# Optimization experiments

Measured on AMD Instinct MI355X. Metric: run time of the kernel, lower is better.

Reference implementation:

```python
import jax, jax.numpy as jnp
import numpy as np
from jax import lax

B, L, C, H, W = 4, 64, 64, 32, 32
K = 3
CONN = 4


def _conv(x, w, b):
    # x: (N, C_in, H, W), w: (C_out, C_in, K, K) -- stride 1, pad K//2 (same as nn.Conv2d)
    p = K // 2
    y = lax.conv_general_dilated(x, w, window_strides=(1, 1), padding=[(p, p), (p, p)],
                                 dimension_numbers=("NCHW", "OIHW", "NCHW"))
    return y + b[None, :, None, None]


def _neighbours_sum(n, m):
    # n: (B*L, C, H, W); m: (B, L, L) bool adjacency with CONN True per row.
    # Equivalent to masked_select + view(B,L,CONN,C,H,W).sum(2): a masked neighbor sum.
    nb = n.reshape(B, L, C, H, W)
    o = jnp.einsum("bij,bjchw->bichw", m.astype(n.dtype), nb)
    return o.reshape(B * L, C, H, W)


def setup_inputs() -> dict:
    key = jax.random.key(0)
    ks = jax.random.split(key, 9)
    fan0 = 1.0 / np.sqrt(C * K * K)
    x = jax.random.normal(ks[0], (B * L, C, H, W), dtype=jnp.float32)
    w_x0 = jax.random.uniform(ks[1], (C, C, K, K), jnp.float32, -fan0, fan0)
    b_x0 = jax.random.uniform(ks[2], (C,), jnp.float32, -fan0, fan0)
    w_n0 = jax.random.uniform(ks[3], (C, C, K, K), jnp.float32, -fan0, fan0)
    b_n0 = jax.random.uniform(ks[4], (C,), jnp.float32, -fan0, fan0)
    w_x1 = jax.random.uniform(ks[5], (C, C, K, K), jnp.float32, -fan0, fan0)
    b_x1 = jax.random.uniform(ks[6], (C,), jnp.float32, -fan0, fan0)
    w_n1 = jax.random.uniform(ks[7], (C, C, K, K), jnp.float32, -fan0, fan0)
    b_n1 = jax.random.uniform(ks[8], (C,), jnp.float32, -fan0, fan0)
    # adjacency with exactly CONN neighbors per (b, i) row
    rng = np.random.default_rng(0)
    idx = np.argsort(rng.random((B, L, L)), axis=-1)[..., :CONN]
    mask = np.zeros((B, L, L), dtype=bool)
    np.put_along_axis(mask, idx, True, axis=-1)
    return {"x": x, "w_x0": w_x0, "b_x0": b_x0, "w_n0": w_n0, "b_n0": b_n0,
            "w_x1": w_x1, "b_x1": b_x1, "w_n1": w_n1, "b_n1": b_n1,
            "neighbours_matrix": jnp.asarray(mask), "connected_num": 4}


def reference(x, w_x0, b_x0, w_n0, b_n0, w_x1, b_x1, w_n1, b_n1, neighbours_matrix, connected_num):
    residual = x
    n_set = _conv(x, w_n0, b_n0)
    h = _conv(x, w_x0, b_x0)
    h = jax.nn.relu(h + _neighbours_sum(n_set, neighbours_matrix))
    n_set = _conv(h, w_n1, b_n1)
    h2 = _conv(h, w_x1, b_x1)
    h2 = h2 + _neighbours_sum(n_set, neighbours_matrix)
    return jax.nn.relu(h2 + residual)
```

## Files before the change

### kernel.cpp

```cpp
#include <hip/hip_runtime.h>

#define NIMG 256
#define CCH 64
#define HWSZ 1024
#define IMG_NHWC 65536

typedef __attribute__((ext_vector_type(8))) short  s16x8;
typedef __attribute__((ext_vector_type(4))) short  s16x4;
typedef __attribute__((ext_vector_type(4))) float  f32x4;

__device__ __forceinline__ unsigned short f2bf(float f) {
    unsigned u = __builtin_bit_cast(unsigned, f);
    u += 0x7fffu + ((u >> 16) & 1u);
    return (unsigned short)(u >> 16);
}
__device__ __forceinline__ float bf2f(unsigned short h) {
    unsigned u = ((unsigned)h) << 16;
    return __builtin_bit_cast(float, u);
}

__device__ __forceinline__ void gload_lds16(const void* g, void* l) {
    __builtin_amdgcn_global_load_lds(
        (const __attribute__((address_space(1))) unsigned int*)g,
        (__attribute__((address_space(3))) unsigned int*)l, 16, 0, 0);
}

__global__ __launch_bounds__(256) void build_nbr_kernel(const unsigned char* __restrict__ mraw,
                                                        int* __restrict__ nbr) {
    __shared__ int nz;
    int t = threadIdx.x;
    if (t == 0) nz = 0;
    __syncthreads();
    int local = 0;
    for (int i = t; i < 16384; i += 256) local += (mraw[i] != 0) ? 1 : 0;
    atomicAdd(&nz, local);
    __syncthreads();
    bool isByte = (nz == 1024);
    const int* mi = (const int*)mraw;
    int c = 0;
    int base = t * 64;
    for (int j = 0; j < 64; ++j) {
        int v = isByte ? (int)mraw[base + j] : mi[base + j];
        if (v != 0 && c < 4) { nbr[t * 4 + c] = j; ++c; }
    }
    for (; c < 4; ++c) nbr[t * 4 + c] = -1;
}

__global__ __launch_bounds__(256) void pack_w_kernel(const float* __restrict__ w0,
                                                     const float* __restrict__ w1,
                                                     const float* __restrict__ w2,
                                                     const float* __restrict__ w3,
                                                     unsigned short* __restrict__ wp) {
    int idx = blockIdx.x * 256 + threadIdx.x;
    if (idx >= 147456) return;
    int e  = idx & 7;
    int sp = (idx >> 3) & 7;
    int co = (idx >> 6) & 63;
    int tc = idx >> 12;
    int cv = tc / 9, tap = tc - cv * 9;
    int ci = ((sp ^ (co & 7)) << 3) + e;
    const float* w = (cv == 0) ? w0 : (cv == 1) ? w1 : (cv == 2) ? w2 : w3;
    wp[idx] = f2bf(w[(co * 64 + ci) * 9 + tap]);
}

__global__ __launch_bounds__(256) void to_nhwc_kernel(const float* __restrict__ x,
                                                      unsigned short* __restrict__ xb) {
    __shared__ unsigned short lds[256 * 68];
    int bid = blockIdx.x;
    int n = bid >> 2, px0 = (bid & 3) * 256;
    int t = threadIdx.x, w = t >> 6, l = t & 63;

    #pragma unroll
    for (int pp = 0; pp < 8; ++pp) {
        int c = w * 16 + pp * 2;
        const float* s0 = x + ((size_t)(n * 64 + c)) * HWSZ + px0;
        const float* s1 = s0 + HWSZ;
        #pragma unroll
        for (int ch = 0; ch < 4; ++ch) {
            int px = ch * 64 + l;
            unsigned pack = (unsigned)f2bf(s0[px]) | ((unsigned)f2bf(s1[px]) << 16);
            *(unsigned*)((char*)lds + px * 136 + c * 2) = pack;
        }
    }
    __syncthreads();
    #pragma unroll
    for (int it = 0; it < 8; ++it) {
        int pos = it * 256 + t;
        int px = pos >> 3, c0 = (pos & 7) * 8;
        const char* src = (const char*)lds + px * 136 + c0 * 2;
        s16x4 v0 = *(const s16x4*)src;
        s16x4 v1 = *(const s16x4*)(src + 8);
        unsigned short* dst = xb + ((size_t)(n * 1024) + px0 + px) * 64 + c0;
        *(s16x4*)dst = v0;
        *(s16x4*)(dst + 4) = v1;
    }
}

__global__ __launch_bounds__(256, 1) void conv_mfma_kernel(const unsigned short* __restrict__ act,
                                                           const unsigned short* __restrict__ wconv,
                                                           const float* __restrict__ bias,
                                                           unsigned short* __restrict__ outp) {
    __shared__ unsigned short wlds[36864];
    __shared__ unsigned short inb[2][10 * 34 * 64];
    int n = blockIdx.x;
    int t = threadIdx.x, w = t >> 6, l = t & 63;

    const unsigned short* img = act + ((size_t)n << 16);
    int x1 = (t >> 3) & 31, slot = t & 7;
    int c = x1 + 1;
    int sslot = slot ^ (c & 7);

    #pragma unroll
    for (int j = 0; j < 18; ++j) {
        int off = j * 4096 + w * 1024;
        gload_lds16((const char*)wconv + off + l * 16, (char*)wlds + off);
    }
    {
        char* ldsbase = (char*)inb[0] + (w * 8 + 1) * 128;
        #pragma unroll
        for (int r = 0; r < 10; ++r) {
            int y = -1 + r;
            if (y >= 0) {
                gload_lds16(img + (y * 32 + x1) * 64 + sslot * 8, ldsbase + r * 4352);
            } else {
                s16x8 z = {0,0,0,0,0,0,0,0};
                *(s16x8*)((char*)inb[0] + r * 4352 + c * 128 + slot * 16) = z;
            }
        }
        if (t < 160) {
            int r = t >> 4, cp = ((t >> 3) & 1) ? 33 : 0, sl = t & 7;
            s16x8 z = {0,0,0,0,0,0,0,0};
            int off = ((r * 34 + cp) * 128 + sl * 16) ^ ((cp & 7) << 4);
            *(s16x8*)((char*)inb[0] + off) = z;
            *(s16x8*)((char*)inb[1] + off) = z;
        }
    }
    __syncthreads();

    int lm = l & 15, kg = l >> 4;

    #pragma unroll
    for (int s = 0; s < 4; ++s) {
        if (s < 3) {
            int y0n = (s + 1) * 8;
            char* ldsbase = (char*)inb[(s + 1) & 1] + (w * 8 + 1) * 128;
            #pragma unroll
            for (int r = 0; r < 10; ++r) {
                int y = y0n - 1 + r;
                if (y < 32) {
                    gload_lds16(img + (y * 32 + x1) * 64 + sslot * 8, ldsbase + r * 4352);
                } else {
                    s16x8 z = {0,0,0,0,0,0,0,0};
                    *(s16x8*)((char*)inb[(s + 1) & 1] + r * 4352 + c * 128 + slot * 16) = z;
                }
            }
        }

        const char* tile = (const char*)inb[s & 1];
        f32x4 acc[4][4];
        #pragma unroll
        for (int m = 0; m < 4; ++m)
            #pragma unroll
            for (int p = 0; p < 4; ++p) acc[m][p] = (f32x4){0.f, 0.f, 0.f, 0.f};

        #pragma unroll
        for (int tap = 0; tap < 9; ++tap) {
            const int dy = tap / 3, dx = tap % 3;
            #pragma unroll
            for (int g = 0; g < 2; ++g) {
                s16x8 a[4], bfr[4];
                #pragma unroll
                for (int m = 0; m < 4; ++m) {
                    int row = m * 16 + lm;
                    int ao  = tap * 8192 + row * 128 + (((g * 4 + kg) ^ (lm & 7)) * 16);
                    a[m] = *(const s16x8*)((const char*)wlds + ao);
                }
                #pragma unroll
                for (int p = 0; p < 4; ++p) {
                    int r  = 2 * w + (p >> 1) + dy;
                    int xl = (p & 1) * 16 + lm + dx;
                    int lb = (r * 4352 + xl * 128 + g * 64 + kg * 16) ^ ((xl & 7) << 4);
                    bfr[p] = *(const s16x8*)(tile + lb);
                }
                #pragma unroll
                for (int m = 0; m < 4; ++m)
                    #pragma unroll
                    for (int p = 0; p < 4; ++p)
                        acc[m][p] = __builtin_amdgcn_mfma_f32_16x16x32_bf16(a[m], bfr[p], acc[m][p], 0, 0, 0);
            }
        }

        int y0 = s * 8;
        #pragma unroll
        for (int m = 0; m < 4; ++m) {
            f32x4 bv = *(const f32x4*)(bias + m * 16 + kg * 4);
            #pragma unroll
            for (int p = 0; p < 4; ++p) {
                int y  = y0 + 2 * w + (p >> 1);
                int xx = (p & 1) * 16 + lm;
                s16x4 o;
                #pragma unroll
                for (int j = 0; j < 4; ++j) o[j] = (short)f2bf(acc[m][p][j] + bv[j]);
                *(s16x4*)(outp + (((size_t)n * 1024 + y * 32 + xx) * 64) + m * 16 + kg * 4) = o;
            }
        }
        if (s < 3) __syncthreads();
    }
}

__global__ __launch_bounds__(256) void agg_relu_kernel(unsigned short* __restrict__ hx,
                                                       const unsigned short* __restrict__ nset,
                                                       const int* __restrict__ nbr) {
    int bid = blockIdx.x;
    int n = bid >> 5;
    int b = n >> 6;
    int rem = ((bid & 31) << 8) + threadIdx.x;
    size_t u = (((size_t)n) << 13) + rem;
    s16x8 hv = *(const s16x8*)(hx + u * 8);
    float s[8];
    #pragma unroll
    for (int j = 0; j < 8; ++j) s[j] = bf2f((unsigned short)hv[j]);
    #pragma unroll
    for (int k = 0; k < 4; ++k) {
        int jn = nbr[n * 4 + k];
        if (jn >= 0) {
            s16x8 nv = *(const s16x8*)(nset + ((((size_t)(b * 64 + jn)) << 13) + rem) * 8);
            #pragma unroll
            for (int j = 0; j < 8; ++j) s[j] += bf2f((unsigned short)nv[j]);
        }
    }
    s16x8 o;
    #pragma unroll
    for (int j = 0; j < 8; ++j) o[j] = (short)f2bf(fmaxf(s[j], 0.f));
    *(s16x8*)(hx + u * 8) = o;
}

__global__ __launch_bounds__(256) void final_kernel(const unsigned short* __restrict__ h2x,
                                                    const unsigned short* __restrict__ nset,
                                                    const int* __restrict__ nbr,
                                                    const float* __restrict__ x,
                                                    float* __restrict__ out) {
    __shared__ float lds[128 * 68];
    int bid = blockIdx.x;
    int n = bid >> 3, px0 = (bid & 7) * 128;
    int b = n >> 6;
    int t = threadIdx.x;
    int j0 = nbr[n * 4 + 0], j1 = nbr[n * 4 + 1], j2 = nbr[n * 4 + 2], j3 = nbr[n * 4 + 3];
    size_t base = ((size_t)n * 1024 + px0) * 64;
    size_t nb[4];
    nb[0] = ((size_t)(b * 64 + (j0 < 0 ? 0 : j0)) * 1024 + px0) * 64;
    nb[1] = ((size_t)(b * 64 + (j1 < 0 ? 0 : j1)) * 1024 + px0) * 64;
    nb[2] = ((size_t)(b * 64 + (j2 < 0 ? 0 : j2)) * 1024 + px0) * 64;
    nb[3] = ((size_t)(b * 64 + (j3 < 0 ? 0 : j3)) * 1024 + px0) * 64;
    int use[4] = {j0 >= 0, j1 >= 0, j2 >= 0, j3 >= 0};

    #pragma unroll
    for (int it = 0; it < 4; ++it) {
        int pos = it * 256 + t;
        int px = pos >> 3, c0 = (pos & 7) * 8;
        int off = px * 64 + c0;
        float s[8];
        s16x8 hv = *(const s16x8*)(h2x + base + off);
        #pragma unroll
        for (int j = 0; j < 8; ++j) s[j] = bf2f((unsigned short)hv[j]);
        #pragma unroll
        for (int k = 0; k < 4; ++k) {
            if (use[k]) {
                s16x8 nv = *(const s16x8*)(nset + nb[k] + off);
                #pragma unroll
                for (int j = 0; j < 8; ++j) s[j] += bf2f((unsigned short)nv[j]);
            }
        }
        float* dst = &lds[px * 68 + c0];
        *(f32x4*)dst = (f32x4){s[0], s[1], s[2], s[3]};
        *(f32x4*)(dst + 4) = (f32x4){s[4], s[5], s[6], s[7]};
    }
    __syncthreads();

    int w = t >> 6, l = t & 63;
    #pragma unroll
    for (int q = 0; q < 4; ++q) {
        int c0 = w * 16 + q * 4;
        #pragma unroll
        for (int half = 0; half < 2; ++half) {
            int px = half * 64 + l;
            f32x4 v = *(const f32x4*)&lds[px * 68 + c0];
            #pragma unroll
            for (int j = 0; j < 4; ++j) {
                size_t a = ((size_t)(n * 64) + c0 + j) * HWSZ + px0 + px;
                out[a] = fmaxf(v[j] + x[a], 0.f);
            }
        }
    }
}

extern "C" void kernel_launch(void* const* d_in, const int* in_sizes, int n_in,
                              void* d_out, int out_size, void* d_ws, size_t ws_size,
                              hipStream_t stream) {
    const float* x    = (const float*)d_in[0];
    const float* w_x0 = (const float*)d_in[1];
    const float* b_x0 = (const float*)d_in[2];
    const float* w_n0 = (const float*)d_in[3];
    const float* b_n0 = (const float*)d_in[4];
    const float* w_x1 = (const float*)d_in[5];
    const float* b_x1 = (const float*)d_in[6];
    const float* w_n1 = (const float*)d_in[7];
    const float* b_n1 = (const float*)d_in[8];
    const unsigned char* mask = (const unsigned char*)d_in[9];

    unsigned short* xb    = (unsigned short*)d_ws;
    unsigned short* hxb   = xb  + (size_t)NIMG * IMG_NHWC;
    unsigned short* nsetb = hxb + (size_t)NIMG * IMG_NHWC;
    unsigned short* wpack = nsetb + (size_t)NIMG * IMG_NHWC;
    int* nbr = (int*)(wpack + 147456);

    build_nbr_kernel<<<1, 256, 0, stream>>>(mask, nbr);
    pack_w_kernel<<<576, 256, 0, stream>>>(w_n0, w_x0, w_n1, w_x1, wpack);
    to_nhwc_kernel<<<1024, 256, 0, stream>>>(x, xb);

    const unsigned short* wp_n0 = wpack;
    const unsigned short* wp_x0 = wpack + 36864;
    const unsigned short* wp_n1 = wpack + 73728;
    const unsigned short* wp_x1 = wpack + 110592;

    conv_mfma_kernel<<<256, 256, 0, stream>>>(xb, wp_n0, b_n0, nsetb);
    conv_mfma_kernel<<<256, 256, 0, stream>>>(xb, wp_x0, b_x0, hxb);
    agg_relu_kernel<<<8192, 256, 0, stream>>>(hxb, nsetb, nbr);

    conv_mfma_kernel<<<256, 256, 0, stream>>>(hxb, wp_n1, b_n1, nsetb);
    conv_mfma_kernel<<<256, 256, 0, stream>>>(hxb, wp_x1, b_x1, xb);
    final_kernel<<<2048, 256, 0, stream>>>(xb, nsetb, nbr, x, (float*)d_out);
}
```

Baseline: 318.8 us.

## Merge conv pairs into one launch split by half-image, restage aggregation through LDS

Each layer's two convolutions run in a single launch with four times as many blocks, each handling a 16-row half image for one weight set, to fill more compute units. Neighbour aggregation now loads all 64 images' slices into LDS once per batch slice. The final kernel takes the residual from the bf16 NHWC copy instead of fp32 x. Weight packing and neighbour-list building share one launch. Halo rows are loaded twice and the bf16 residual reduces precision.

```diff
diff --git a/kernel.cpp b/kernel.cpp
--- a/kernel.cpp
+++ b/kernel.cpp
@@ -25,34 +25,34 @@
         (__attribute__((address_space(3))) unsigned int*)l, 16, 0, 0);
 }
 
-__global__ __launch_bounds__(256) void build_nbr_kernel(const unsigned char* __restrict__ mraw,
-                                                        int* __restrict__ nbr) {
-    __shared__ int nz;
-    int t = threadIdx.x;
-    if (t == 0) nz = 0;
-    __syncthreads();
-    int local = 0;
-    for (int i = t; i < 16384; i += 256) local += (mraw[i] != 0) ? 1 : 0;
-    atomicAdd(&nz, local);
-    __syncthreads();
-    bool isByte = (nz == 1024);
-    const int* mi = (const int*)mraw;
-    int c = 0;
-    int base = t * 64;
-    for (int j = 0; j < 64; ++j) {
-        int v = isByte ? (int)mraw[base + j] : mi[base + j];
-        if (v != 0 && c < 4) { nbr[t * 4 + c] = j; ++c; }
-    }
-    for (; c < 4; ++c) nbr[t * 4 + c] = -1;
-}
-
-__global__ __launch_bounds__(256) void pack_w_kernel(const float* __restrict__ w0,
-                                                     const float* __restrict__ w1,
-                                                     const float* __restrict__ w2,
-                                                     const float* __restrict__ w3,
-                                                     unsigned short* __restrict__ wp) {
+__global__ __launch_bounds__(256) void pack_build_kernel(const float* __restrict__ w0,
+                                                         const float* __restrict__ w1,
+                                                         const float* __restrict__ w2,
+                                                         const float* __restrict__ w3,
+                                                         unsigned short* __restrict__ wp,
+                                                         const unsigned char* __restrict__ mraw,
+                                                         int* __restrict__ nbr) {
+    if (blockIdx.x == 576) {
+        __shared__ int nz;
+        int t = threadIdx.x;
+        if (t == 0) nz = 0;
+        __syncthreads();
+        int local = 0;
+        for (int i = t; i < 16384; i += 256) local += (mraw[i] != 0) ? 1 : 0;
+        atomicAdd(&nz, local);
+        __syncthreads();
+        bool isByte = (nz == 1024);
+        const int* mi = (const int*)mraw;
+        int c = 0;
+        int base = t * 64;
+        for (int j = 0; j < 64; ++j) {
+            int v = isByte ? (int)mraw[base + j] : mi[base + j];
+            if (v != 0 && c < 4) { nbr[t * 4 + c] = j; ++c; }
+        }
+        for (; c < 4; ++c) nbr[t * 4 + c] = -1;
+        return;
+    }
     int idx = blockIdx.x * 256 + threadIdx.x;
-    if (idx >= 147456) return;
     int e  = idx & 7;
     int sp = (idx >> 3) & 7;
     int co = (idx >> 6) & 63;
@@ -96,19 +96,22 @@
     }
 }
 
-__global__ __launch_bounds__(256, 1) void conv_mfma_kernel(const unsigned short* __restrict__ act,
-                                                           const unsigned short* __restrict__ wconv,
-                                                           const float* __restrict__ bias,
-                                                           unsigned short* __restrict__ outp) {
+__global__ __launch_bounds__(256, 1) void conv_pair_kernel(const unsigned short* __restrict__ act,
+                                                           const unsigned short* __restrict__ wpA,
+                                                           const unsigned short* __restrict__ wpB,
+                                                           const float* __restrict__ bA,
+                                                           const float* __restrict__ bB,
+                                                           unsigned short* __restrict__ outA,
+                                                           unsigned short* __restrict__ outB) {
     __shared__ unsigned short wlds[36864];
-    __shared__ unsigned short inb[2][10 * 34 * 64];
-    int n = blockIdx.x;
+    __shared__ unsigned short tile[18 * 34 * 64];
+    int bid = blockIdx.x;
+    int n = bid >> 2, half = (bid >> 1) & 1, sel = bid & 1;
+    const unsigned short* wconv = sel ? wpB : wpA;
+    const float* bias = sel ? bB : bA;
+    unsigned short* outp = sel ? outB : outA;
+    int y0 = half * 16;
     int t = threadIdx.x, w = t >> 6, l = t & 63;
-
-    const unsigned short* img = act + ((size_t)n << 16);
-    int x1 = (t >> 3) & 31, slot = t & 7;
-    int c = x1 + 1;
-    int sslot = slot ^ (c & 7);
 
     #pragma unroll
     for (int j = 0; j < 18; ++j) {
@@ -116,129 +119,147 @@
         gload_lds16((const char*)wconv + off + l * 16, (char*)wlds + off);
     }
     {
-        char* ldsbase = (char*)inb[0] + (w * 8 + 1) * 128;
-        #pragma unroll
-        for (int r = 0; r < 10; ++r) {
-            int y = -1 + r;
-            if (y >= 0) {
-                gload_lds16(img + (y * 32 + x1) * 64 + sslot * 8, ldsbase + r * 4352);
+        const unsigned short* img = act + ((size_t)n << 16);
+        int x1 = (t >> 3) & 31, slot = t & 7;
+        int c = x1 + 1;
+        int sslot = slot ^ (c & 7);
+        char* base = (char*)tile + 128 + w * 1024;
+        #pragma unroll
+        for (int r = 0; r < 18; ++r) {
+            int y = y0 - 1 + r;
+            if (y >= 0 && y < 32) {
+                gload_lds16(img + (y * 32 + x1) * 64 + sslot * 8, base + r * 4352);
             } else {
                 s16x8 z = {0,0,0,0,0,0,0,0};
-                *(s16x8*)((char*)inb[0] + r * 4352 + c * 128 + slot * 16) = z;
-            }
-        }
-        if (t < 160) {
-            int r = t >> 4, cp = ((t >> 3) & 1) ? 33 : 0, sl = t & 7;
-            s16x8 z = {0,0,0,0,0,0,0,0};
-            int off = ((r * 34 + cp) * 128 + sl * 16) ^ ((cp & 7) << 4);
-            *(s16x8*)((char*)inb[0] + off) = z;
-            *(s16x8*)((char*)inb[1] + off) = z;
+                *(s16x8*)((char*)tile + r * 4352 + c * 128 + slot * 16) = z;
+            }
+        }
+        #pragma unroll
+        for (int k = 0; k < 2; ++k) {
+            int idx = k * 256 + t;
+            if (idx < 288) {
+                int r = idx >> 4, cp = ((idx >> 3) & 1) ? 33 : 0, sl = idx & 7;
+                s16x8 z = {0,0,0,0,0,0,0,0};
+                int off = ((r * 34 + cp) * 128 + sl * 16) ^ ((cp & 7) << 4);
+                *(s16x8*)((char*)tile + off) = z;
+            }
         }
     }
     __syncthreads();
 
     int lm = l & 15, kg = l >> 4;
-
-    #pragma unroll
-    for (int s = 0; s < 4; ++s) {
-        if (s < 3) {
-            int y0n = (s + 1) * 8;
-            char* ldsbase = (char*)inb[(s + 1) & 1] + (w * 8 + 1) * 128;
-            #pragma unroll
-            for (int r = 0; r < 10; ++r) {
-                int y = y0n - 1 + r;
-                if (y < 32) {
-                    gload_lds16(img + (y * 32 + x1) * 64 + sslot * 8, ldsbase + r * 4352);
-                } else {
-                    s16x8 z = {0,0,0,0,0,0,0,0};
-                    *(s16x8*)((char*)inb[(s + 1) & 1] + r * 4352 + c * 128 + slot * 16) = z;
+    f32x4 acc[4][8];
+    #pragma unroll
+    for (int m = 0; m < 4; ++m)
+        #pragma unroll
+        for (int p = 0; p < 8; ++p) acc[m][p] = (f32x4){0.f, 0.f, 0.f, 0.f};
+
+    #pragma unroll
+    for (int tap = 0; tap < 9; ++tap) {
+        const int dy = tap / 3, dx = tap % 3;
+        #pragma unroll
+        for (int g = 0; g < 2; ++g) {
+            s16x8 a[4];
+            #pragma unroll
+            for (int m = 0; m < 4; ++m) {
+                int row = m * 16 + lm;
+                int ao  = tap * 8192 + row * 128 + (((g * 4 + kg) ^ (lm & 7)) * 16);
+                a[m] = *(const s16x8*)((const char*)wlds + ao);
+            }
+            #pragma unroll
+            for (int rl = 0; rl < 4; ++rl) {
+                int r = 4 * w + rl + dy;
+                s16x8 b0, b1;
+                {
+                    int xl = lm + dx;
+                    int lb = (r * 4352 + xl * 128 + g * 64 + kg * 16) ^ ((xl & 7) << 4);
+                    b0 = *(const s16x8*)((const char*)tile + lb);
                 }
-            }
-        }
-
-        const char* tile = (const char*)inb[s & 1];
-        f32x4 acc[4][4];
-        #pragma unroll
-        for (int m = 0; m < 4; ++m)
-            #pragma unroll
-            for (int p = 0; p < 4; ++p) acc[m][p] = (f32x4){0.f, 0.f, 0.f, 0.f};
-
-        #pragma unroll
-        for (int tap = 0; tap < 9; ++tap) {
-            const int dy = tap / 3, dx = tap % 3;
-            #pragma unroll
-            for (int g = 0; g < 2; ++g) {
-                s16x8 a[4], bfr[4];
+                {
+                    int xl = 16 + lm + dx;
+                    int lb = (r * 4352 + xl * 128 + g * 64 + kg * 16) ^ ((xl & 7) << 4);
+                    b1 = *(const s16x8*)((const char*)tile + lb);
+                }
                 #pragma unroll
                 for (int m = 0; m < 4; ++m) {
-                    int row = m * 16 + lm;
-                    int ao  = tap * 8192 + row * 128 + (((g * 4 + kg) ^ (lm & 7)) * 16);
-                    a[m] = *(const s16x8*)((const char*)wlds + ao);
+                    acc[m][rl * 2 + 0] = __builtin_amdgcn_mfma_f32_16x16x32_bf16(a[m], b0, acc[m][rl * 2 + 0], 0, 0, 0);
+                    acc[m][rl * 2 + 1] = __builtin_amdgcn_mfma_f32_16x16x32_bf16(a[m], b1, acc[m][rl * 2 + 1], 0, 0, 0);
                 }
-                #pragma unroll
-                for (int p = 0; p < 4; ++p) {
-                    int r  = 2 * w + (p >> 1) + dy;
-                    int xl = (p & 1) * 16 + lm + dx;
-                    int lb = (r * 4352 + xl * 128 + g * 64 + kg * 16) ^ ((xl & 7) << 4);
-                    bfr[p] = *(const s16x8*)(tile + lb);
-                }
-                #pragma unroll
-                for (int m = 0; m < 4; ++m)
-                    #pragma unroll
-                    for (int p = 0; p < 4; ++p)
-                        acc[m][p] = __builtin_amdgcn_mfma_f32_16x16x32_bf16(a[m], bfr[p], acc[m][p], 0, 0, 0);
-            }
-        }
-
-        int y0 = s * 8;
-        #pragma unroll
-        for (int m = 0; m < 4; ++m) {
-            f32x4 bv = *(const f32x4*)(bias + m * 16 + kg * 4);
-            #pragma unroll
-            for (int p = 0; p < 4; ++p) {
-                int y  = y0 + 2 * w + (p >> 1);
-                int xx = (p & 1) * 16 + lm;
+            }
+        }
+    }
+
+    #pragma unroll
+    for (int m = 0; m < 4; ++m) {
+        f32x4 bv = *(const f32x4*)(bias + m * 16 + kg * 4);
+        #pragma unroll
+        for (int rl = 0; rl < 4; ++rl) {
+            int y = y0 + 4 * w + rl;
+            #pragma unroll
+            for (int ph = 0; ph < 2; ++ph) {
+                int xx = ph * 16 + lm;
                 s16x4 o;
                 #pragma unroll
-                for (int j = 0; j < 4; ++j) o[j] = (short)f2bf(acc[m][p][j] + bv[j]);
+                for (int j = 0; j < 4; ++j) o[j] = (short)f2bf(acc[m][rl * 2 + ph][j] + bv[j]);
                 *(s16x4*)(outp + (((size_t)n * 1024 + y * 32 + xx) * 64) + m * 16 + kg * 4) = o;
             }
         }
-        if (s < 3) __syncthreads();
-    }
-}
-
-__global__ __launch_bounds__(256) void agg_relu_kernel(unsigned short* __restrict__ hx,
-                                                       const unsigned short* __restrict__ nset,
-                                                       const int* __restrict__ nbr) {
+    }
+}
+
+__global__ __launch_bounds__(256, 2) void agg_relu2_kernel(unsigned short* __restrict__ hx,
+                                                           const unsigned short* __restrict__ nset,
+                                                           const int* __restrict__ nbr) {
+    __shared__ unsigned short lds[64 * 65 * 8];
     int bid = blockIdx.x;
-    int n = bid >> 5;
-    int b = n >> 6;
-    int rem = ((bid & 31) << 8) + threadIdx.x;
-    size_t u = (((size_t)n) << 13) + rem;
-    s16x8 hv = *(const s16x8*)(hx + u * 8);
-    float s[8];
-    #pragma unroll
-    for (int j = 0; j < 8; ++j) s[j] = bf2f((unsigned short)hv[j]);
-    #pragma unroll
-    for (int k = 0; k < 4; ++k) {
-        int jn = nbr[n * 4 + k];
-        if (jn >= 0) {
-            s16x8 nv = *(const s16x8*)(nset + ((((size_t)(b * 64 + jn)) << 13) + rem) * 8);
-            #pragma unroll
-            for (int j = 0; j < 8; ++j) s[j] += bf2f((unsigned short)nv[j]);
-        }
-    }
-    s16x8 o;
-    #pragma unroll
-    for (int j = 0; j < 8; ++j) o[j] = (short)f2bf(fmaxf(s[j], 0.f));
-    *(s16x8*)(hx + u * 8) = o;
+    int b = bid >> 7, sl = bid & 127;
+    size_t base_e = (size_t)sl * 512;
+    int t = threadIdx.x, w = t >> 6, l = t & 63;
+
+    #pragma unroll
+    for (int k = 0; k < 16; ++k) {
+        int j = w * 16 + k;
+        gload_lds16(nset + (((size_t)(b * 64 + j)) << 16) + base_e + l * 8,
+                    (char*)lds + j * 1040 + l * 16);
+    }
+    __syncthreads();
+
+    int i = t >> 2, q = t & 3;
+    int j0 = nbr[(b * 64 + i) * 4 + 0];
+    int j1 = nbr[(b * 64 + i) * 4 + 1];
+    int j2 = nbr[(b * 64 + i) * 4 + 2];
+    int j3 = nbr[(b * 64 + i) * 4 + 3];
+    unsigned short* row = hx + (((size_t)(b * 64 + i)) << 16) + base_e + q * 128;
+    #pragma unroll
+    for (int u = 0; u < 16; ++u) {
+        int e = q * 16 + u;
+        s16x8 hv = *(const s16x8*)(row + u * 8);
+        float s[8];
+        #pragma unroll
+        for (int j = 0; j < 8; ++j) s[j] = bf2f((unsigned short)hv[j]);
+        if (j0 >= 0) { s16x8 nv = *(const s16x8*)((const char*)lds + (j0 * 65 + e) * 16);
+            #pragma unroll
+            for (int j = 0; j < 8; ++j) s[j] += bf2f((unsigned short)nv[j]); }
+        if (j1 >= 0) { s16x8 nv = *(const s16x8*)((const char*)lds + (j1 * 65 + e) * 16);
+            #pragma unroll
+            for (int j = 0; j < 8; ++j) s[j] += bf2f((unsigned short)nv[j]); }
+        if (j2 >= 0) { s16x8 nv = *(const s16x8*)((const char*)lds + (j2 * 65 + e) * 16);
+            #pragma unroll
+            for (int j = 0; j < 8; ++j) s[j] += bf2f((unsigned short)nv[j]); }
+        if (j3 >= 0) { s16x8 nv = *(const s16x8*)((const char*)lds + (j3 * 65 + e) * 16);
+            #pragma unroll
+            for (int j = 0; j < 8; ++j) s[j] += bf2f((unsigned short)nv[j]); }
+        s16x8 o;
+        #pragma unroll
+        for (int j = 0; j < 8; ++j) o[j] = (short)f2bf(fmaxf(s[j], 0.f));
+        *(s16x8*)(row + u * 8) = o;
+    }
 }
 
 __global__ __launch_bounds__(256) void final_kernel(const unsigned short* __restrict__ h2x,
                                                     const unsigned short* __restrict__ nset,
                                                     const int* __restrict__ nbr,
-                                                    const float* __restrict__ x,
+                                                    const unsigned short* __restrict__ xb,
                                                     float* __restrict__ out) {
     __shared__ float lds[128 * 68];
     int bid = blockIdx.x;
@@ -261,8 +282,10 @@
         int off = px * 64 + c0;
         float s[8];
         s16x8 hv = *(const s16x8*)(h2x + base + off);
-        #pragma unroll
-        for (int j = 0; j < 8; ++j) s[j] = bf2f((unsigned short)hv[j]);
+        s16x8 rv = *(const s16x8*)(xb + base + off);
+        #pragma unroll
+        for (int j = 0; j < 8; ++j)
+            s[j] = bf2f((unsigned short)hv[j]) + bf2f((unsigned short)rv[j]);
         #pragma unroll
         for (int k = 0; k < 4; ++k) {
             if (use[k]) {
@@ -272,8 +295,8 @@
             }
         }
         float* dst = &lds[px * 68 + c0];
-        *(f32x4*)dst = (f32x4){s[0], s[1], s[2], s[3]};
-        *(f32x4*)(dst + 4) = (f32x4){s[4], s[5], s[6], s[7]};
+        *(f32x4*)dst = (f32x4){fmaxf(s[0],0.f), fmaxf(s[1],0.f), fmaxf(s[2],0.f), fmaxf(s[3],0.f)};
+        *(f32x4*)(dst + 4) = (f32x4){fmaxf(s[4],0.f), fmaxf(s[5],0.f), fmaxf(s[6],0.f), fmaxf(s[7],0.f)};
     }
     __syncthreads();
 
@@ -288,7 +311,7 @@
             #pragma unroll
             for (int j = 0; j < 4; ++j) {
                 size_t a = ((size_t)(n * 64) + c0 + j) * HWSZ + px0 + px;
-                out[a] = fmaxf(v[j] + x[a], 0.f);
+                out[a] = v[j];
             }
         }
     }
@@ -309,13 +332,13 @@
     const unsigned char* mask = (const unsigned char*)d_in[9];
 
     unsigned short* xb    = (unsigned short*)d_ws;
-    unsigned short* hxb   = xb  + (size_t)NIMG * IMG_NHWC;
-    unsigned short* nsetb = hxb + (size_t)NIMG * IMG_NHWC;
-    unsigned short* wpack = nsetb + (size_t)NIMG * IMG_NHWC;
+    unsigned short* hxb   = xb   + (size_t)NIMG * IMG_NHWC;
+    unsigned short* nsetb = hxb  + (size_t)NIMG * IMG_NHWC;
+    unsigned short* h2xb  = nsetb + (size_t)NIMG * IMG_NHWC;
+    unsigned short* wpack = h2xb + (size_t)NIMG * IMG_NHWC;
     int* nbr = (int*)(wpack + 147456);
 
-    build_nbr_kernel<<<1, 256, 0, stream>>>(mask, nbr);
-    pack_w_kernel<<<576, 256, 0, stream>>>(w_n0, w_x0, w_n1, w_x1, wpack);
+    pack_build_kernel<<<577, 256, 0, stream>>>(w_n0, w_x0, w_n1, w_x1, wpack, mask, nbr);
     to_nhwc_kernel<<<1024, 256, 0, stream>>>(x, xb);
 
     const unsigned short* wp_n0 = wpack;
@@ -323,11 +346,9 @@
     const unsigned short* wp_n1 = wpack + 73728;
     const unsigned short* wp_x1 = wpack + 110592;
 
-    conv_mfma_kernel<<<256, 256, 0, stream>>>(xb, wp_n0, b_n0, nsetb);
-    conv_mfma_kernel<<<256, 256, 0, stream>>>(xb, wp_x0, b_x0, hxb);
-    agg_relu_kernel<<<8192, 256, 0, stream>>>(hxb, nsetb, nbr);
-
-    conv_mfma_kernel<<<256, 256, 0, stream>>>(hxb, wp_n1, b_n1, nsetb);
-    conv_mfma_kernel<<<256, 256, 0, stream>>>(hxb, wp_x1, b_x1, xb);
-    final_kernel<<<2048, 256, 0, stream>>>(xb, nsetb, nbr, x, (float*)d_out);
-}
+    conv_pair_kernel<<<1024, 256, 0, stream>>>(xb, wp_n0, wp_x0, b_n0, b_x0, nsetb, hxb);
+    agg_relu2_kernel<<<512, 256, 0, stream>>>(hxb, nsetb, nbr);
+
+    conv_pair_kernel<<<1024, 256, 0, stream>>>(hxb, wp_n1, wp_x1, b_n1, b_x1, nsetb, h2xb);
+    final_kernel<<<2048, 256, 0, stream>>>(h2xb, nsetb, nbr, xb, (float*)d_out);
+}
```

New measurement: 344.9 us. 1.08x slower.
